# Performance work log

Measured on AMD Instinct MI355X. Metric: run time of the kernel, lower is better.

## Reference

```python
import jax, jax.numpy as jnp
import numpy as np

HIDDEN = 1024
NUM_HEADS = 16
HEAD_DIM = HIDDEN // NUM_HEADS


def rotate_half(x):
    x1, x2 = jnp.split(x, 2, axis=-1)
    return jnp.concatenate((-x2, x1), axis=-1)


def rope_tables(T, dim, dtype):
    inv_freq = 1.0 / (10000.0 ** (jnp.arange(0, dim, 2, dtype=jnp.float32) / dim))
    t = jnp.arange(T, dtype=jnp.float32)
    freqs = t[:, None] * inv_freq[None, :]           # [T, dim/2]
    emb = jnp.concatenate((freqs, freqs), axis=-1)   # [T, dim]
    return jnp.cos(emb).astype(dtype), jnp.sin(emb).astype(dtype)


def setup_inputs() -> dict:
    key = jax.random.key(0)
    kx, kq, kk, kv, ko = jax.random.split(key, 5)
    B, T = 2, 2048
    scale = 1.0 / np.sqrt(HIDDEN)
    return {
        "x": jax.random.normal(kx, (B, T, HIDDEN), dtype=jnp.float32),
        "wq": jax.random.normal(kq, (HIDDEN, HIDDEN), dtype=jnp.float32) * scale,
        "wk": jax.random.normal(kk, (HIDDEN, HIDDEN), dtype=jnp.float32) * scale,
        "wv": jax.random.normal(kv, (HIDDEN, HIDDEN), dtype=jnp.float32) * scale,
        "wo": jax.random.normal(ko, (HIDDEN, HIDDEN), dtype=jnp.float32) * scale,
    }


def reference(x, wq, wk, wv, wo):
    B, T, _ = x.shape
    H, D = NUM_HEADS, HEAD_DIM
    # projections (Linear, no bias): x @ W.T; reshape to [B, H, T, D]
    q = (x @ wq.T).reshape(B, T, H, D).transpose(0, 2, 1, 3)
    k = (x @ wk.T).reshape(B, T, H, D).transpose(0, 2, 1, 3)
    v = (x @ wv.T).reshape(B, T, H, D).transpose(0, 2, 1, 3)
    cos, sin = rope_tables(T, D, x.dtype)            # [T, D]
    cos = cos[None, None]                            # [1,1,T,D]
    sin = sin[None, None]
    q = q * cos + rotate_half(q) * sin
    k = k * cos + rotate_half(k) * sin
    scores = jnp.einsum("bhtd,bhsd->bhts", q, k) / np.sqrt(D).astype(x.dtype)
    attn = jax.nn.softmax(scores, axis=-1)
    out = jnp.einsum("bhts,bhsd->bhtd", attn, v)     # [B,H,T,D]
    out = out.transpose(0, 2, 1, 3).reshape(B, T, H * D)
    return out @ wo.T
```

## Files before the change

### kernel.cpp

```cpp
#include <hip/hip_runtime.h>
#include <hip/hip_bf16.h>
#include <stdint.h>

typedef __bf16 bf16;
typedef __attribute__((ext_vector_type(8))) __bf16 bf16x8;
typedef __attribute__((ext_vector_type(4))) float f32x4;
typedef __attribute__((ext_vector_type(16))) float f32x16;

#define L2E 1.4426950408889634f

__device__ __forceinline__ f32x4 mfma16(bf16x8 a, bf16x8 b, f32x4 c) {
  return __builtin_amdgcn_mfma_f32_16x16x32_bf16(a, b, c, 0, 0, 0);
}

__device__ __forceinline__ f32x16 mfma32(bf16x8 a, bf16x8 b, f32x16 c) {
  return __builtin_amdgcn_mfma_f32_32x32x16_bf16(a, b, c, 0, 0, 0);
}

__device__ __forceinline__ void gload16(void* lds, const void* g) {
  __builtin_amdgcn_global_load_lds(
      (const __attribute__((address_space(1))) uint32_t*)g,
      (__attribute__((address_space(3))) uint32_t*)lds, 16, 0, 0);
}

__device__ __forceinline__ unsigned cvt_pk_bf16(float lo, float hi) {
  unsigned r;
  asm("v_cvt_pk_bf16_f32 %0, %1, %2" : "=v"(r) : "v"(lo), "v"(hi));
  return r;
}

__device__ __forceinline__ void pl32swap(unsigned& a, unsigned& b) {
  auto r = __builtin_amdgcn_permlane32_swap(a, b, false, false);
  a = r[0];
  b = r[1];
}

__global__ __launch_bounds__(256) void prep_cast(
    const float* __restrict__ x, const float* __restrict__ wq,
    const float* __restrict__ wk, const float* __restrict__ wv,
    const float* __restrict__ wo, bf16* __restrict__ xb,
    bf16* __restrict__ wqb, bf16* __restrict__ wkb, bf16* __restrict__ wvb,
    bf16* __restrict__ wob) {
  int i = blockIdx.x * 256 + threadIdx.x;
  const int NX = 4096 * 1024 / 4;
  const int NW = 1024 * 1024 / 4;
  const float* src; bf16* dst; int off;
  if (i < NX)               { src = x;  dst = xb;  off = i; }
  else if (i < NX + NW)     { src = wq; dst = wqb; off = i - NX; }
  else if (i < NX + 2 * NW) { src = wk; dst = wkb; off = i - (NX + NW); }
  else if (i < NX + 3 * NW) { src = wv; dst = wvb; off = i - (NX + 2 * NW); }
  else                      { src = wo; dst = wob; off = i - (NX + 3 * NW); }
  float4 v = ((const float4*)src)[off];
  union { bf16 h[4]; uint2 u; } o;
  o.h[0] = (bf16)v.x; o.h[1] = (bf16)v.y; o.h[2] = (bf16)v.z; o.h[3] = (bf16)v.w;
  ((uint2*)dst)[off] = o.u;
}

__global__ __launch_bounds__(256) void rope_tab(float* __restrict__ ct,
                                                float* __restrict__ st) {
  int i = blockIdx.x * 256 + threadIdx.x;
  int t = i >> 5, d = i & 31;
  float inv = powf(10000.f, -(float)d * (1.f / 32.f));
  float a = (float)t * inv;
  ct[i] = cosf(a);
  st[i] = sinf(a);
}

__device__ __forceinline__ void gemm_mainloop(const bf16* __restrict__ A,
                                              const bf16* __restrict__ W,
                                              int m0, int n0,
                                              bf16 (*As)[4096], bf16 (*Bs)[4096],
                                              f32x4 acc[4][4]) {
  const int tid = threadIdx.x;
  const int lane = tid & 63, wave = tid >> 6;
  const int wr = (wave >> 1) * 64, wc = (wave & 1) * 64;
  const int lr = lane & 15, lh = lane >> 4;

  auto stage = [&](bf16* dA, bf16* dB, int kt) {
    int k0 = kt * 32;
#pragma unroll
    for (int p = 0; p < 2; p++) {
      int u = p * 256 + tid; int row = u >> 2; int kg = (u & 3) ^ (row & 3);
      gload16(dA + (size_t)u * 8, A + (size_t)(m0 + row) * 1024 + k0 + kg * 8);
    }
#pragma unroll
    for (int p = 0; p < 2; p++) {
      int u = p * 256 + tid; int row = u >> 2; int kg = (u & 3) ^ (row & 3);
      gload16(dB + (size_t)u * 8, W + (size_t)(n0 + row) * 1024 + k0 + kg * 8);
    }
  };

  stage(As[0], Bs[0], 0);
  int cur = 0;
  for (int kt = 0; kt < 32; ++kt) {
    __syncthreads();
    const bf16* cA = As[cur]; const bf16* cB = Bs[cur];
    bf16x8 af[4], bfr[4];
#pragma unroll
    for (int i = 0; i < 4; i++) {
      int row = wr + i * 16 + lr; int un = row * 4 + (lh ^ (row & 3));
      af[i] = *(const bf16x8*)(cA + (size_t)un * 8);
    }
#pragma unroll
    for (int j = 0; j < 4; j++) {
      int row = wc + j * 16 + lr; int un = row * 4 + (lh ^ (row & 3));
      bfr[j] = *(const bf16x8*)(cB + (size_t)un * 8);
    }
    if (kt + 1 < 32) stage(As[cur ^ 1], Bs[cur ^ 1], kt + 1);
#pragma unroll
    for (int i = 0; i < 4; i++)
#pragma unroll
      for (int j = 0; j < 4; j++) acc[i][j] = mfma16(af[i], bfr[j], acc[i][j]);
    cur ^= 1;
  }
}

__global__ __launch_bounds__(256) void gemm_qkv(
    const bf16* __restrict__ xb, const bf16* __restrict__ wq,
    const bf16* __restrict__ wk, const bf16* __restrict__ wv,
    const float* __restrict__ ct, const float* __restrict__ st,
    bf16* __restrict__ qo, bf16* __restrict__ ko, bf16* __restrict__ vo) {
  __shared__ __align__(16) bf16 As[2][4096];
  __shared__ __align__(16) bf16 Bs[2][4096];
  int bm = blockIdx.x, bn = blockIdx.y;
  int proj = bn >> 3;
  const bf16* W = proj == 0 ? wq : (proj == 1 ? wk : wv);
  bf16* out = proj == 0 ? qo : (proj == 1 ? ko : vo);
  int m0 = bm * 128, n0 = (bn & 7) * 128;

  f32x4 zero = {0.f, 0.f, 0.f, 0.f};
  f32x4 acc[4][4];
#pragma unroll
  for (int i = 0; i < 4; i++)
#pragma unroll
    for (int j = 0; j < 4; j++) acc[i][j] = zero;

  gemm_mainloop(xb, W, m0, n0, As, Bs, acc);

  const int tid = threadIdx.x, lane = tid & 63, wave = tid >> 6;
  const int wr = (wave >> 1) * 64, wc = (wave & 1) * 64;
  const int lr = lane & 15, lh = lane >> 4;
  int colb = n0 + wc;
  int h = colb >> 6;
  const float QSC = 0.125f * L2E;
#pragma unroll
  for (int i = 0; i < 4; i++) {
#pragma unroll
    for (int r = 0; r < 4; r++) {
      int m = m0 + wr + i * 16 + lh * 4 + r;
      int b = m >> 11, t = m & 2047;
      float v0 = acc[i][0][r], v1 = acc[i][1][r];
      float v2 = acc[i][2][r], v3 = acc[i][3][r];
      if (proj < 2) {
        float c0 = ct[t * 32 + lr],      s0 = st[t * 32 + lr];
        float c1 = ct[t * 32 + 16 + lr], s1 = st[t * 32 + 16 + lr];
        float n0v = v0 * c0 - v2 * s0, n2 = v2 * c0 + v0 * s0;
        float n1 = v1 * c1 - v3 * s1,  n3 = v3 * c1 + v1 * s1;
        v0 = n0v; v1 = n1; v2 = n2; v3 = n3;
        if (proj == 0) { v0 *= QSC; v1 *= QSC; v2 *= QSC; v3 *= QSC; }
      }
      size_t base = ((size_t)(b * 16 + h) * 2048 + t) * 64;
      out[base + lr]      = (bf16)v0;
      out[base + 16 + lr] = (bf16)v1;
      out[base + 32 + lr] = (bf16)v2;
      out[base + 48 + lr] = (bf16)v3;
    }
  }
}

__global__ __launch_bounds__(256) void vtrans(const bf16* __restrict__ v,
                                              bf16* __restrict__ vt) {
  __shared__ bf16 tile[64][68];
  int bh = blockIdx.x, tt = blockIdx.y;
  int tid = threadIdx.x;
  const bf16* src = v + ((size_t)bh * 2048 + tt * 64) * 64;
  int rr0 = tid >> 4;
  int c4 = (tid & 15) * 4;
#pragma unroll
  for (int p = 0; p < 4; p++) {
    int r = p * 16 + rr0;
    *(uint2*)&tile[r][c4] = *(const uint2*)(src + (size_t)r * 64 + c4);
  }
  __syncthreads();
  bf16* dst = vt + (size_t)bh * 64 * 2048 + tt * 64;
#pragma unroll
  for (int p = 0; p < 4; p++) {
    int d = p * 16 + rr0;
    union { bf16 h[4]; uint2 u; } o;
#pragma unroll
    for (int q = 0; q < 4; q++) o.h[q] = tile[c4 + q][d];
    *(uint2*)(dst + (size_t)d * 2048 + c4) = o.u;
  }
}

__global__ __launch_bounds__(128, 2) void attn(const bf16* __restrict__ q,
                                               const bf16* __restrict__ k,
                                               const bf16* __restrict__ vt,
                                               bf16* __restrict__ o) {
  __shared__ __align__(16) bf16 smem[2][2][64][64];
  char* smb = (char*)&smem[0][0][0][0];
  int p = blockIdx.x;
  int L = (p & 7) * 128 + (p >> 3);
  int bh = L >> 5, qt = L & 31;

  const int tid = threadIdx.x, lane = tid & 63, wave = tid >> 6;
  const int lq = lane & 31, hi = lane >> 5;

  const bf16* kg = k + (size_t)bh * 2048 * 64;
  const bf16* vg = vt + (size_t)bh * 64 * 2048;

  int q0 = qt * 64 + wave * 32;
  const bf16* qb = q + ((size_t)bh * 2048 + q0) * 64;
  bf16x8 qf[4];
#pragma unroll
  for (int kk = 0; kk < 4; kk++)
    qf[kk] = *(const bf16x8*)(qb + (size_t)lq * 64 + kk * 16 + hi * 8);

  int va[4];
#pragma unroll
  for (int j = 0; j < 4; j++)
    va[j] = lq * 128 + (((2 * j + hi) ^ (lq & 7)) << 4);

  int koffe[4], voffe[4];
#pragma unroll
  for (int pp = 0; pp < 4; pp++) {
    int uu = pp * 128 + tid;
    int r = uu >> 3;
    int u = (uu & 7) ^ (r & 7);
    koffe[pp] = r * 64 + u * 8;
    voffe[pp] = r * 2048 + u * 8;
  }

  f32x16 acc[2];
  f32x16 CM;
#pragma unroll
  for (int r = 0; r < 16; r++) { acc[0][r] = 0.f; acc[1][r] = 0.f; CM[r] = -16.f; }
  float l = 0.f;

  auto stage = [&](int bufoff, int it) {
#pragma unroll
    for (int pp = 0; pp < 4; pp++) {
      int uu = pp * 128 + tid;
      gload16(smb + bufoff + uu * 16, kg + it * 4096 + koffe[pp]);
      gload16(smb + bufoff + 8192 + uu * 16, vg + it * 64 + voffe[pp]);
    }
  };

  auto compute = [&](int bufoff) {
#pragma unroll
    for (int c = 0; c < 2; c++) {
      __builtin_amdgcn_s_setprio(1);
      f32x16 s = mfma32(*(const bf16x8*)(smb + bufoff + c * 4096 + va[0]),
                        qf[0], CM);
#pragma unroll
      for (int kk = 1; kk < 4; kk++)
        s = mfma32(*(const bf16x8*)(smb + bufoff + c * 4096 + va[kk]),
                   qf[kk], s);
      __builtin_amdgcn_s_setprio(0);

      float su0 = 0.f, su1 = 0.f;
      unsigned pk[8];
#pragma unroll
      for (int i = 0; i < 8; i++) {
        float pa = __builtin_amdgcn_exp2f(s[2 * i]);
        float pb2 = __builtin_amdgcn_exp2f(s[2 * i + 1]);
        su0 += pa;
        su1 += pb2;
        pk[i] = cvt_pk_bf16(pa, pb2);
      }
      l += su0 + su1;

      pl32swap(pk[0], pk[2]);
      pl32swap(pk[1], pk[3]);
      pl32swap(pk[4], pk[6]);
      pl32swap(pk[5], pk[7]);
      __builtin_amdgcn_s_setprio(1);
#pragma unroll
      for (int cc = 0; cc < 2; cc++) {
        union { unsigned u[4]; bf16x8 v; } pb;
        pb.u[0] = pk[4 * cc + 0];
        pb.u[1] = pk[4 * cc + 1];
        pb.u[2] = pk[4 * cc + 2];
        pb.u[3] = pk[4 * cc + 3];
#pragma unroll
        for (int db = 0; db < 2; db++) {
          bf16x8 va8 = *(const bf16x8*)(smb + bufoff + 8192 + db * 4096 +
                                        va[2 * c + cc]);
          acc[db] = mfma32(va8, pb.v, acc[db]);
        }
      }
      __builtin_amdgcn_s_setprio(0);
    }
  };

  stage(0, 0);
  __syncthreads();

  for (int it2 = 0; it2 < 16; ++it2) {
    stage(16384, 2 * it2 + 1);
    compute(0);
    __syncthreads();
    if (it2 + 1 < 16) stage(0, 2 * it2 + 2);
    compute(16384);
    __syncthreads();
  }

  {
    unsigned ta = __float_as_uint(l), tb = ta;
    pl32swap(ta, tb);
    l = __uint_as_float(ta) + __uint_as_float(tb);
  }
  float inv = 1.0f / l;
  int b = bh >> 4, h = bh & 15;
  int qrow = q0 + lq;
  bf16* orow = o + ((size_t)(b * 2048 + qrow)) * 1024 + h * 64;
#pragma unroll
  for (int db = 0; db < 2; db++)
#pragma unroll
    for (int g = 0; g < 4; g++) {
      union { bf16 h4[4]; uint2 u; } t;
#pragma unroll
      for (int e = 0; e < 4; e++) t.h4[e] = (bf16)(acc[db][4 * g + e] * inv);
      *(uint2*)(orow + db * 32 + 8 * g + 4 * hi) = t.u;
    }
}

__global__ __launch_bounds__(256) void gemm_out(const bf16* __restrict__ ab,
                                                const bf16* __restrict__ wo,
                                                float* __restrict__ out) {
  __shared__ __align__(16) bf16 As[2][4096];
  __shared__ __align__(16) bf16 Bs[2][4096];
  int m0 = blockIdx.x * 128, n0 = blockIdx.y * 128;
  f32x4 zero = {0.f, 0.f, 0.f, 0.f};
  f32x4 acc[4][4];
#pragma unroll
  for (int i = 0; i < 4; i++)
#pragma unroll
    for (int j = 0; j < 4; j++) acc[i][j] = zero;

  gemm_mainloop(ab, wo, m0, n0, As, Bs, acc);

  const int tid = threadIdx.x, lane = tid & 63, wave = tid >> 6;
  const int wr = (wave >> 1) * 64, wc = (wave & 1) * 64;
  const int lr = lane & 15, lh = lane >> 4;
#pragma unroll
  for (int i = 0; i < 4; i++)
#pragma unroll
    for (int r = 0; r < 4; r++) {
      int m = m0 + wr + i * 16 + lh * 4 + r;
#pragma unroll
      for (int j = 0; j < 4; j++) {
        int col = n0 + wc + j * 16 + lr;
        out[(size_t)m * 1024 + col] = acc[i][j][r];
      }
    }
}

extern "C" void kernel_launch(void* const* d_in, const int* in_sizes, int n_in,
                              void* d_out, int out_size, void* d_ws, size_t ws_size,
                              hipStream_t stream) {
  const float* x  = (const float*)d_in[0];
  const float* wq = (const float*)d_in[1];
  const float* wk = (const float*)d_in[2];
  const float* wv = (const float*)d_in[3];
  const float* wo = (const float*)d_in[4];
  float* out = (float*)d_out;
  char* ws = (char*)d_ws;
  const size_t MB = 1u << 20;
  bf16* xb  = (bf16*)(ws + 0);
  bf16* wqb = (bf16*)(ws + 8 * MB);
  bf16* wkb = (bf16*)(ws + 10 * MB);
  bf16* wvb = (bf16*)(ws + 12 * MB);
  bf16* wob = (bf16*)(ws + 14 * MB);
  bf16* qw  = (bf16*)(ws + 16 * MB);
  bf16* kw  = (bf16*)(ws + 24 * MB);
  bf16* vw  = (bf16*)(ws + 32 * MB);
  bf16* vtw = (bf16*)(ws + 40 * MB);
  bf16* aw  = (bf16*)(ws + 48 * MB);
  float* ct = (float*)(ws + 56 * MB);
  float* st = (float*)(ws + 56 * MB + 256 * 1024);

  prep_cast<<<8192, 256, 0, stream>>>(x, wq, wk, wv, wo, xb, wqb, wkb, wvb, wob);
  rope_tab<<<256, 256, 0, stream>>>(ct, st);
  gemm_qkv<<<dim3(32, 24), 256, 0, stream>>>(xb, wqb, wkb, wvb, ct, st, qw, kw, vw);
  vtrans<<<dim3(32, 32), 256, 0, stream>>>(vw, vtw);
  attn<<<1024, 128, 0, stream>>>(qw, kw, vtw, aw);
  gemm_out<<<dim3(32, 8), 256, 0, stream>>>(aw, wob, out);
}
```

Before: 119.7 us.

## Split attention key range across two wave pairs and merge partial results

Measured after the change: 121.1 us. About the same (+1.1%).

```diff
diff --git a/kernel.cpp b/kernel.cpp
--- a/kernel.cpp
+++ b/kernel.cpp
@@ -193,42 +193,48 @@
   }
 }
 
-__global__ __launch_bounds__(128, 2) void attn(const bf16* __restrict__ q,
+__global__ __launch_bounds__(256, 4) void attn(const bf16* __restrict__ q,
                                                const bf16* __restrict__ k,
                                                const bf16* __restrict__ vt,
                                                bf16* __restrict__ o) {
-  __shared__ __align__(16) bf16 smem[2][2][64][64];
-  char* smb = (char*)&smem[0][0][0][0];
-  int p = blockIdx.x;
-  int L = (p & 7) * 128 + (p >> 3);
+  __shared__ __align__(16) char smb[32768];
+  int pidx = blockIdx.x;
+  int L = (pidx & 7) * 128 + (pidx >> 3);
   int bh = L >> 5, qt = L & 31;
 
   const int tid = threadIdx.x, lane = tid & 63, wave = tid >> 6;
   const int lq = lane & 31, hi = lane >> 5;
+  const int p = wave >> 1;
+  const int sub = wave & 1;
+  const int t128 = tid & 127;
 
   const bf16* kg = k + (size_t)bh * 2048 * 64;
   const bf16* vg = vt + (size_t)bh * 64 * 2048;
 
-  int q0 = qt * 64 + wave * 32;
+  int q0 = qt * 64 + sub * 32;
   const bf16* qb = q + ((size_t)bh * 2048 + q0) * 64;
   bf16x8 qf[4];
 #pragma unroll
   for (int kk = 0; kk < 4; kk++)
     qf[kk] = *(const bf16x8*)(qb + (size_t)lq * 64 + kk * 16 + hi * 8);
 
-  int va[4];
+  int vaK[4];
 #pragma unroll
   for (int j = 0; j < 4; j++)
-    va[j] = lq * 128 + (((2 * j + hi) ^ (lq & 7)) << 4);
-
-  int koffe[4], voffe[4];
-#pragma unroll
-  for (int pp = 0; pp < 4; pp++) {
-    int uu = pp * 128 + tid;
-    int r = uu >> 3;
-    int u = (uu & 7) ^ (r & 7);
-    koffe[pp] = r * 64 + u * 8;
-    voffe[pp] = r * 2048 + u * 8;
+    vaK[j] = lq * 128 + (((2 * j + hi) ^ (lq & 7)) << 4);
+  int vaV[2];
+#pragma unroll
+  for (int cc = 0; cc < 2; cc++)
+    vaV[cc] = lq * 64 + (((2 * cc + hi) ^ (lq & 3)) << 4) + 4096;
+
+  int koffe[2], voffe[2];
+#pragma unroll
+  for (int pp = 0; pp < 2; pp++) {
+    int uu = pp * 128 + t128;
+    int rK = uu >> 3, uK = (uu & 7) ^ (rK & 7);
+    koffe[pp] = rK * 64 + uK * 8;
+    int rV = uu >> 2, uV = (uu & 3) ^ (rV & 3);
+    voffe[pp] = rV * 2048 + uV * 8;
   }
 
   f32x16 acc[2];
@@ -237,73 +243,85 @@
   for (int r = 0; r < 16; r++) { acc[0][r] = 0.f; acc[1][r] = 0.f; CM[r] = -16.f; }
   float l = 0.f;
 
-  auto stage = [&](int bufoff, int it) {
-#pragma unroll
-    for (int pp = 0; pp < 4; pp++) {
-      int uu = pp * 128 + tid;
-      gload16(smb + bufoff + uu * 16, kg + it * 4096 + koffe[pp]);
-      gload16(smb + bufoff + 8192 + uu * 16, vg + it * 64 + voffe[pp]);
+  const int sbase = p * 16384;
+  auto stage = [&](int bufoff, int itl) {
+    const bf16* kt = kg + p * 65536 + itl * 2048;
+    const bf16* vt2 = vg + p * 1024 + itl * 32;
+#pragma unroll
+    for (int pp = 0; pp < 2; pp++) {
+      gload16(smb + bufoff + (pp * 128 + t128) * 16, kt + koffe[pp]);
+      gload16(smb + bufoff + 4096 + (pp * 128 + t128) * 16, vt2 + voffe[pp]);
     }
   };
 
   auto compute = [&](int bufoff) {
-#pragma unroll
-    for (int c = 0; c < 2; c++) {
-      __builtin_amdgcn_s_setprio(1);
-      f32x16 s = mfma32(*(const bf16x8*)(smb + bufoff + c * 4096 + va[0]),
-                        qf[0], CM);
-#pragma unroll
-      for (int kk = 1; kk < 4; kk++)
-        s = mfma32(*(const bf16x8*)(smb + bufoff + c * 4096 + va[kk]),
-                   qf[kk], s);
-      __builtin_amdgcn_s_setprio(0);
-
-      float su0 = 0.f, su1 = 0.f;
-      unsigned pk[8];
-#pragma unroll
-      for (int i = 0; i < 8; i++) {
-        float pa = __builtin_amdgcn_exp2f(s[2 * i]);
-        float pb2 = __builtin_amdgcn_exp2f(s[2 * i + 1]);
-        su0 += pa;
-        su1 += pb2;
-        pk[i] = cvt_pk_bf16(pa, pb2);
+    __builtin_amdgcn_s_setprio(1);
+    f32x16 s = mfma32(*(const bf16x8*)(smb + bufoff + vaK[0]), qf[0], CM);
+#pragma unroll
+    for (int kk = 1; kk < 4; kk++)
+      s = mfma32(*(const bf16x8*)(smb + bufoff + vaK[kk]), qf[kk], s);
+    __builtin_amdgcn_s_setprio(0);
+
+    float su0 = 0.f, su1 = 0.f;
+    unsigned pk[8];
+#pragma unroll
+    for (int i = 0; i < 8; i++) {
+      float pa = __builtin_amdgcn_exp2f(s[2 * i]);
+      float pb2 = __builtin_amdgcn_exp2f(s[2 * i + 1]);
+      su0 += pa;
+      su1 += pb2;
+      pk[i] = cvt_pk_bf16(pa, pb2);
+    }
+    l += su0 + su1;
+
+    pl32swap(pk[0], pk[2]);
+    pl32swap(pk[1], pk[3]);
+    pl32swap(pk[4], pk[6]);
+    pl32swap(pk[5], pk[7]);
+    __builtin_amdgcn_s_setprio(1);
+#pragma unroll
+    for (int cc = 0; cc < 2; cc++) {
+      union { unsigned u[4]; bf16x8 v; } pb;
+      pb.u[0] = pk[4 * cc + 0];
+      pb.u[1] = pk[4 * cc + 1];
+      pb.u[2] = pk[4 * cc + 2];
+      pb.u[3] = pk[4 * cc + 3];
+#pragma unroll
+      for (int db = 0; db < 2; db++) {
+        bf16x8 va8 = *(const bf16x8*)(smb + bufoff + db * 2048 + vaV[cc]);
+        acc[db] = mfma32(va8, pb.v, acc[db]);
       }
-      l += su0 + su1;
-
-      pl32swap(pk[0], pk[2]);
-      pl32swap(pk[1], pk[3]);
-      pl32swap(pk[4], pk[6]);
-      pl32swap(pk[5], pk[7]);
-      __builtin_amdgcn_s_setprio(1);
-#pragma unroll
-      for (int cc = 0; cc < 2; cc++) {
-        union { unsigned u[4]; bf16x8 v; } pb;
-        pb.u[0] = pk[4 * cc + 0];
-        pb.u[1] = pk[4 * cc + 1];
-        pb.u[2] = pk[4 * cc + 2];
-        pb.u[3] = pk[4 * cc + 3];
-#pragma unroll
-        for (int db = 0; db < 2; db++) {
-          bf16x8 va8 = *(const bf16x8*)(smb + bufoff + 8192 + db * 4096 +
-                                        va[2 * c + cc]);
-          acc[db] = mfma32(va8, pb.v, acc[db]);
-        }
-      }
-      __builtin_amdgcn_s_setprio(0);
-    }
+    }
+    __builtin_amdgcn_s_setprio(0);
   };
 
-  stage(0, 0);
+  stage(sbase, 0);
   __syncthreads();
 
-  for (int it2 = 0; it2 < 16; ++it2) {
-    stage(16384, 2 * it2 + 1);
-    compute(0);
+  for (int it = 0; it < 32; ++it) {
+    if (it + 1 < 32) stage(sbase + ((it + 1) & 1) * 8192, it + 1);
+    compute(sbase + (it & 1) * 8192);
     __syncthreads();
-    if (it2 + 1 < 16) stage(0, 2 * it2 + 2);
-    compute(16384);
-    __syncthreads();
-  }
+  }
+
+  float* mbuf = (float*)(smb + 16384);
+  float* lbuf = (float*)smb;
+  if (p == 1) {
+#pragma unroll
+    for (int db = 0; db < 2; db++)
+#pragma unroll
+      for (int r = 0; r < 16; r++)
+        mbuf[sub * 2048 + (db * 16 + r) * 64 + lane] = acc[db][r];
+    lbuf[sub * 64 + lane] = l;
+  }
+  __syncthreads();
+  if (p == 1) return;
+#pragma unroll
+  for (int db = 0; db < 2; db++)
+#pragma unroll
+    for (int r = 0; r < 16; r++)
+      acc[db][r] += mbuf[sub * 2048 + (db * 16 + r) * 64 + lane];
+  l += lbuf[sub * 64 + lane];
 
   {
     unsigned ta = __float_as_uint(l), tb = ta;
@@ -384,6 +402,6 @@
   rope_tab<<<256, 256, 0, stream>>>(ct, st);
   gemm_qkv<<<dim3(32, 24), 256, 0, stream>>>(xb, wqb, wkb, wvb, ct, st, qw, kw, vw);
   vtrans<<<dim3(32, 32), 256, 0, stream>>>(vw, vtw);
-  attn<<<1024, 128, 0, stream>>>(qw, kw, vtw, aw);
+  attn<<<1024, 256, 0, stream>>>(qw, kw, vtw, aw);
   gemm_out<<<dim3(32, 8), 256, 0, stream>>>(aw, wob, out);
 }
```
